# Kernel optimization log

Hardware: AMD Instinct MI355X
Metric: run time of the kernel (lower is better)

## Reference

```python
import jax, jax.numpy as jnp
import numpy as np

B, S, D, H, DFF = 2, 4096, 256, 8, 1024
DK = D // H


def setup_inputs() -> dict:
    key = jax.random.key(0)
    ks = jax.random.split(key, 12)
    sc = 0.02
    inp = {
        "x": jax.random.normal(ks[0], (B, S, D), jnp.float32),
        "mask": jnp.ones((B, 1, 1, S), jnp.int32),
        "Wq": jax.random.normal(ks[1], (D, D), jnp.float32) * sc,
        "bq": jnp.zeros((D,), jnp.float32),
        "Wk": jax.random.normal(ks[2], (D, D), jnp.float32) * sc,
        "bk": jnp.zeros((D,), jnp.float32),
        "Wv": jax.random.normal(ks[3], (D, D), jnp.float32) * sc,
        "bv": jnp.zeros((D,), jnp.float32),
        "Wo": jax.random.normal(ks[4], (D, D), jnp.float32) * sc,
        "bo": jnp.zeros((D,), jnp.float32),
        "W1": jax.random.normal(ks[5], (D, DFF), jnp.float32) * sc,
        "b1": jnp.zeros((DFF,), jnp.float32),
        "W2": jax.random.normal(ks[6], (DFF, D), jnp.float32) * sc,
        "b2": jnp.zeros((D,), jnp.float32),
        "g1": jnp.ones((D,), jnp.float32),
        "be1": jnp.zeros((D,), jnp.float32),
        "g2": jnp.ones((D,), jnp.float32),
        "be2": jnp.zeros((D,), jnp.float32),
        "a1": jnp.float32(1e-8),
        "a2": jnp.float32(1e-8),
    }
    return inp


def _layernorm(x, g, b, eps=1e-5):
    mu = jnp.mean(x, axis=-1, keepdims=True)
    var = jnp.var(x, axis=-1, keepdims=True)
    return (x - mu) * jax.lax.rsqrt(var + eps) * g + b


def _block(x, mask, Wq, bq, Wk, bk, Wv, bv, Wo, bo, W1, b1, W2, b2, g1, be1, g2, be2, a1, a2):
    # multi-head attention (dropout = identity in eval)
    def proj(W, b):
        return (x @ W + b).reshape(B, S, H, DK).transpose(0, 2, 1, 3)  # [B,H,S,DK]
    q, k, v = proj(Wq, bq), proj(Wk, bk), proj(Wv, bv)
    scores = jnp.einsum("bhsd,bhtd->bhst", q, k) / jnp.sqrt(jnp.float32(DK))
    scores = jnp.where(mask == 0, jnp.float32(-1e9), scores)
    p_attn = jax.nn.softmax(scores, axis=-1)
    ctx = jnp.einsum("bhst,bhtd->bhsd", p_attn, v)
    ctx = ctx.transpose(0, 2, 1, 3).reshape(B, S, D)
    attn_out = ctx @ Wo + bo
    x1 = _layernorm(x + a1 * attn_out, g1, be1)
    # FFN
    h = jax.nn.gelu(x1 @ W1 + b1, approximate=False)
    ffn_out = h @ W2 + b2
    return _layernorm(x1 + a2 * ffn_out, g2, be2)


def reference(x, mask, Wq, bq, Wk, bk, Wv, bv, Wo, bo, W1, b1, W2, b2, g1, be1, g2, be2, a1, a2):
    return _block(x, mask, Wq, bq, Wk, bk, Wv, bv, Wo, bo, W1, b1, W2, b2, g1, be1, g2, be2, a1, a2)
```

## Files before the change

kernel.cpp:

```cpp
#include <hip/hip_runtime.h>
#include <hip/hip_bf16.h>
#include <math.h>

#define B_ 2
#define S_ 4096
#define D_ 256
#define H_ 8
#define DFF_ 1024
#define DK_ 32

typedef __attribute__((ext_vector_type(8))) short short8;
typedef __attribute__((ext_vector_type(4))) float f32x4;
typedef __attribute__((ext_vector_type(16))) float f32x16;
typedef __attribute__((ext_vector_type(4))) int int4v;

__device__ __forceinline__ unsigned short f2bf(float f) {
  unsigned int u = __builtin_bit_cast(unsigned int, f);
  u += 0x7FFFu + ((u >> 16) & 1u);
  return (unsigned short)(u >> 16);
}

__device__ __forceinline__ float bf2f(unsigned short s) {
  unsigned int u = ((unsigned int)s) << 16;
  return __builtin_bit_cast(float, u);
}

__device__ __forceinline__ short8 u32x4_to_s8(unsigned int a, unsigned int b,
                                              unsigned int c, unsigned int d) {
  int4v v = {(int)a, (int)b, (int)c, (int)d};
  return __builtin_bit_cast(short8, v);
}

__global__ __launch_bounds__(256) void k_prepw(
    const float* __restrict__ Wq, const float* __restrict__ Wk,
    const float* __restrict__ Wv, const float* __restrict__ Wo,
    const float* __restrict__ W1, const float* __restrict__ W2,
    const float* __restrict__ bq, const float* __restrict__ bk,
    const float* __restrict__ bv, const float* __restrict__ x,
    unsigned short* __restrict__ WqkvT, unsigned short* __restrict__ WoT,
    unsigned short* __restrict__ W1T, unsigned short* __restrict__ W2T,
    float* __restrict__ bqkv, unsigned short* __restrict__ xb) {
  const float k2 = 0.25500525551f;
  int bx = blockIdx.x, t = threadIdx.x;
  if (bx < 768) {
    int which = bx >> 8;
    int i = ((bx & 255) << 8) | t;
    const float* W = (which == 0) ? Wq : (which == 1) ? Wk : Wv;
    int n = i >> 8, k = i & 255;
    float v = W[k * 256 + n] * ((which == 0) ? k2 : 1.0f);
    WqkvT[(size_t)(which * 256 + n) * 256 + k] = f2bf(v);
  } else if (bx < 1024) {
    int i = ((bx - 768) << 8) | t;
    int n = i >> 8, k = i & 255;
    WoT[i] = f2bf(Wo[k * 256 + n]);
  } else if (bx < 2048) {
    int i = ((bx - 1024) << 8) | t;
    int n = i >> 8, k = i & 255;
    W1T[i] = f2bf(W1[k * 1024 + n]);
  } else if (bx < 3072) {
    int i = ((bx - 2048) << 8) | t;
    int n = i >> 10, k = i & 1023;
    W2T[i] = f2bf(W2[k * 256 + n]);
  } else if (bx < 3075) {
    int i = ((bx - 3072) << 8) | t;
    if (i < 768) bqkv[i] = (i < 256) ? bq[i] * k2 : (i < 512) ? bk[i - 256] : bv[i - 512];
  } else {
    int i = (bx - 3075) * 2048 + t * 8;
    f32x4 f0 = *(const f32x4*)(x + i);
    f32x4 f1 = *(const f32x4*)(x + i + 4);
    short8 o;
#pragma unroll
    for (int e = 0; e < 4; e++) { o[e] = (short)f2bf(f0[e]); o[e + 4] = (short)f2bf(f1[e]); }
    *(short8*)(xb + i) = o;
  }
}

__global__ __launch_bounds__(256) void k_gemmqkv(const unsigned short* __restrict__ A,
                                                 const unsigned short* __restrict__ Bt,
                                                 const float* __restrict__ bias,
                                                 unsigned short* __restrict__ qb,
                                                 unsigned short* __restrict__ kpk,
                                                 unsigned short* __restrict__ vpk) {
  const int K = 256;
  __shared__ unsigned short Al[128][40];
  __shared__ unsigned short Bl[64][40];
  const int tid = threadIdx.x;
  const int wid = tid >> 6, lane = tid & 63;
  const int lhi = lane >> 4, llo = lane & 15;
  const int rowbase = wid * 32;
  const int bm = blockIdx.x, bn = blockIdx.y;

  f32x4 zero = {0.f, 0.f, 0.f, 0.f};
  f32x4 acc[2][4];
#pragma unroll
  for (int m = 0; m < 2; m++)
#pragma unroll
    for (int n = 0; n < 4; n++) acc[m][n] = zero;

  const int r0 = tid >> 2, c8 = (tid & 3) * 8;
  const unsigned short* A16a = A + (size_t)(bm * 128 + r0) * K + c8;
  const unsigned short* A16b = A + (size_t)(bm * 128 + r0 + 64) * K + c8;
  const unsigned short* Brow0 = Bt + (size_t)(bn * 64 + r0) * K + c8;

  for (int kb = 0; kb < K; kb += 32) {
    __syncthreads();
    *(short8*)&Al[r0][c8] = *(const short8*)(A16a + kb);
    *(short8*)&Al[r0 + 64][c8] = *(const short8*)(A16b + kb);
    *(short8*)&Bl[r0][c8] = *(const short8*)(Brow0 + kb);
    __syncthreads();
    short8 af[2], bf[4];
#pragma unroll
    for (int m = 0; m < 2; m++) af[m] = *(const short8*)&Al[rowbase + m * 16 + llo][lhi * 8];
#pragma unroll
    for (int n = 0; n < 4; n++) bf[n] = *(const short8*)&Bl[n * 16 + llo][lhi * 8];
#pragma unroll
    for (int m = 0; m < 2; m++)
#pragma unroll
      for (int n = 0; n < 4; n++)
        acc[m][n] = __builtin_amdgcn_mfma_f32_16x16x32_bf16(af[m], bf[n], acc[m][n], 0, 0, 0);
  }

  const int which = bn >> 2;
#pragma unroll
  for (int m = 0; m < 2; m++)
#pragma unroll
    for (int n = 0; n < 4; n++)
#pragma unroll
      for (int r = 0; r < 4; r++) {
        int row = bm * 128 + rowbase + m * 16 + lhi * 4 + r;
        int gcol = bn * 64 + n * 16 + llo;
        int col0 = gcol - which * 256;
        float v = acc[m][n][r] + bias[gcol];
        unsigned short bv = f2bf(v);
        int t = row & (S_ - 1), b = row >> 12;
        int h = col0 >> 5;
        if (which == 0) {
          qb[(size_t)row * 256 + col0] = bv;
        } else if (which == 1) {
          int c5 = col0 & 31, jj = (c5 >> 4) & 1, hik = (c5 >> 3) & 1, e = c5 & 7;
          int tile = t >> 6, i = (t >> 5) & 1, l31k = t & 31;
          size_t addr = (((size_t)(b * 8 + h) * 64 + tile) * 4 + i * 2 + jj) * 512 +
                        (hik * 32 + l31k) * 8 + e;
          kpk[addr] = bv;
        } else {
          int d = col0 & 31;
          int x5 = t >> 6, j = (t >> 3) & 7, kk = t & 7;
          size_t addr = (((size_t)(b * 8 + h) * 64 + x5) * 4 + (j >> 1)) * 512 +
                        ((j & 1) * 32 + d) * 8 + kk;
          vpk[addr] = bv;
        }
      }
}

__global__ __launch_bounds__(256) void k_gemm1(const unsigned short* __restrict__ A,
                                               const unsigned short* __restrict__ Bt,
                                               const float* __restrict__ bias,
                                               unsigned short* __restrict__ Cout,
                                               int M, int N, int K) {
  __shared__ unsigned short Al[128][40];
  __shared__ unsigned short Bl[128][40];
  const int tid = threadIdx.x;
  const int wid = tid >> 6, lane = tid & 63;
  const int lhi = lane >> 4, llo = lane & 15;
  const int wr = wid >> 1, wc = wid & 1;
  const int rowbase = wr * 64, colbase = wc * 64;
  const int bm = blockIdx.x, bn = blockIdx.y;

  f32x4 zero = {0.f, 0.f, 0.f, 0.f};
  f32x4 acc[4][4];
#pragma unroll
  for (int m = 0; m < 4; m++)
#pragma unroll
    for (int n = 0; n < 4; n++) acc[m][n] = zero;

  const int r0 = tid >> 2, c8 = (tid & 3) * 8;
  const unsigned short* A16a = A + (size_t)(bm * 128 + r0) * K + c8;
  const unsigned short* A16b = A + (size_t)(bm * 128 + r0 + 64) * K + c8;
  const unsigned short* Brow0 = Bt + (size_t)(bn * 128 + r0) * K + c8;
  const unsigned short* Brow1 = Bt + (size_t)(bn * 128 + r0 + 64) * K + c8;

  for (int kb = 0; kb < K; kb += 32) {
    __syncthreads();
    *(short8*)&Al[r0][c8] = *(const short8*)(A16a + kb);
    *(short8*)&Al[r0 + 64][c8] = *(const short8*)(A16b + kb);
    *(short8*)&Bl[r0][c8] = *(const short8*)(Brow0 + kb);
    *(short8*)&Bl[r0 + 64][c8] = *(const short8*)(Brow1 + kb);
    __syncthreads();
    short8 af[4], bf[4];
#pragma unroll
    for (int m = 0; m < 4; m++) af[m] = *(const short8*)&Al[rowbase + m * 16 + llo][lhi * 8];
#pragma unroll
    for (int n = 0; n < 4; n++) bf[n] = *(const short8*)&Bl[colbase + n * 16 + llo][lhi * 8];
#pragma unroll
    for (int m = 0; m < 4; m++)
#pragma unroll
      for (int n = 0; n < 4; n++)
        acc[m][n] = __builtin_amdgcn_mfma_f32_16x16x32_bf16(af[m], bf[n], acc[m][n], 0, 0, 0);
  }

#pragma unroll
  for (int m = 0; m < 4; m++)
#pragma unroll
    for (int n = 0; n < 4; n++)
#pragma unroll
      for (int r = 0; r < 4; r++) {
        int row = bm * 128 + rowbase + m * 16 + lhi * 4 + r;
        int col = bn * 128 + colbase + n * 16 + llo;
        float v = acc[m][n][r] + bias[col];
        v = 0.5f * v * (1.0f + erff(v * 0.70710678118f));
        Cout[(size_t)row * N + col] = f2bf(v);
      }
}

template <int BASE16, int OUT32>
__global__ __launch_bounds__(512) void k_gemmln(const unsigned short* __restrict__ A,
                                                const unsigned short* __restrict__ Bt,
                                                const float* __restrict__ bias,
                                                const void* __restrict__ base,
                                                const float* __restrict__ alpha,
                                                const float* __restrict__ g,
                                                const float* __restrict__ be,
                                                void* __restrict__ y, int K) {
  __shared__ unsigned short Al[2][32][40];
  __shared__ unsigned short Bl[2][256][40];
  __shared__ float psum[32][4], psq[32][4];
  float* partial = (float*)&Bl[0][0][0];

  const int tid = threadIdx.x;
  const int w = tid >> 6, lane = tid & 63;
  const int kh = w >> 2, wc = w & 3;
  const int lhi = lane >> 4, llo = lane & 15;
  const int row0 = blockIdx.x * 32;
  const int Kh = K >> 1;

  f32x4 zero = {0.f, 0.f, 0.f, 0.f};
  f32x4 acc[2][4];
#pragma unroll
  for (int m = 0; m < 2; m++)
#pragma unroll
    for (int n = 0; n < 4; n++) acc[m][n] = zero;

  for (int kb = 0; kb < Kh; kb += 32) {
    __syncthreads();
    if (tid < 256) {
      int kh2 = tid >> 7, ra = (tid >> 2) & 31, ca = (tid & 3) * 8;
      *(short8*)&Al[kh2][ra][ca] =
          *(const short8*)(A + (size_t)(row0 + ra) * K + kh2 * Kh + kb + ca);
    }
#pragma unroll
    for (int s = 0; s < 4; s++) {
      int c = tid + s * 512;
      int kh2 = c >> 10, rb = (c >> 2) & 255, cb = (c & 3) * 8;
      *(short8*)&Bl[kh2][rb][cb] =
          *(const short8*)(Bt + (size_t)rb * K + kh2 * Kh + kb + cb);
    }
    __syncthreads();
    short8 af[2], bf[4];
#pragma unroll
    for (int m = 0; m < 2; m++) af[m] = *(const short8*)&Al[kh][m * 16 + llo][lhi * 8];
#pragma unroll
    for (int n = 0; n < 4; n++)
      bf[n] = *(const short8*)&Bl[kh][wc * 64 + n * 16 + llo][lhi * 8];
#pragma unroll
    for (int m = 0; m < 2; m++)
#pragma unroll
      for (int n = 0; n < 4; n++)
        acc[m][n] = __builtin_amdgcn_mfma_f32_16x16x32_bf16(af[m], bf[n], acc[m][n], 0, 0, 0);
  }

  __syncthreads();
  if (kh == 1) {
#pragma unroll
    for (int m = 0; m < 2; m++)
#pragma unroll
      for (int n = 0; n < 4; n++)
#pragma unroll
        for (int r = 0; r < 4; r++) {
          int lrow = m * 16 + lhi * 4 + r;
          int col = wc * 64 + n * 16 + llo;
          partial[lrow * 256 + col] = acc[m][n][r];
        }
  }
  __syncthreads();

  const float a = alpha[0];
  const unsigned short* b16 = (const unsigned short*)base;
  const float* b32 = (const float*)base;

  if (kh == 0) {
#pragma unroll
    for (int m = 0; m < 2; m++)
#pragma unroll
      for (int r = 0; r < 4; r++) {
        int lrow = m * 16 + lhi * 4 + r;
        size_t grow = (size_t)(row0 + lrow);
        float s = 0.f, q = 0.f;
#pragma unroll
        for (int n = 0; n < 4; n++) {
          int col = wc * 64 + n * 16 + llo;
          float v = acc[m][n][r] + partial[lrow * 256 + col] + bias[col];
          float xb = BASE16 ? bf2f(b16[grow * 256 + col]) : b32[grow * 256 + col];
          float rr = fmaf(a, v, xb);
          acc[m][n][r] = rr;
          s += rr;
          q = fmaf(rr, rr, q);
        }
#pragma unroll
        for (int off = 1; off < 16; off <<= 1) {
          s += __shfl_xor(s, off);
          q += __shfl_xor(q, off);
        }
        if (llo == 0) { psum[lrow][wc] = s; psq[lrow][wc] = q; }
      }
  }
  __syncthreads();

  if (kh == 0) {
#pragma unroll
    for (int m = 0; m < 2; m++)
#pragma unroll
      for (int r = 0; r < 4; r++) {
        int lrow = m * 16 + lhi * 4 + r;
        size_t grow = (size_t)(row0 + lrow);
        float S = psum[lrow][0] + psum[lrow][1] + psum[lrow][2] + psum[lrow][3];
        float Q = psq[lrow][0] + psq[lrow][1] + psq[lrow][2] + psq[lrow][3];
        float mu = S * (1.0f / 256.0f);
        float var = Q * (1.0f / 256.0f) - mu * mu;
        float rs = rsqrtf(var + 1e-5f);
#pragma unroll
        for (int n = 0; n < 4; n++) {
          int col = wc * 64 + n * 16 + llo;
          float o = (acc[m][n][r] - mu) * rs * g[col] + be[col];
          if (OUT32) ((float*)y)[grow * 256 + col] = o;
          else ((unsigned short*)y)[grow * 256 + col] = f2bf(o);
        }
      }
  }
}

__global__ __launch_bounds__(512, 2) void k_attn(const unsigned short* __restrict__ qb,
                                                 const unsigned short* __restrict__ kpk,
                                                 const unsigned short* __restrict__ vpk,
                                                 const int* __restrict__ mask,
                                                 unsigned short* __restrict__ ctx) {
  __shared__ float accS[4][32][32];
  __shared__ float lS[4][32];
  const int tid = threadIdx.x;
  const int lane = tid & 63;
  const int w = tid >> 6;
  const int qt = w >> 1, half = w & 1;
  const int l31 = lane & 31, hi = lane >> 5;
  const int q0 = blockIdx.x * 128 + qt * 32;
  const int h = blockIdx.y, b = blockIdx.z;
  const size_t bS = (size_t)b * S_;

  const unsigned short* Qp = qb + (bS + q0 + l31) * 256 + h * DK_ + hi * 8;
  short8 qf0 = *(const short8*)Qp;
  short8 qf1 = *(const short8*)(Qp + 16);

  const size_t fragbase = ((size_t)(b * H_ + h) * 64 + half * 32) * 2048 + lane * 8;
  const unsigned short* kp = kpk + fragbase;
  const unsigned short* vp = vpk + fragbase;
  const int* mp = mask + bS + half * 2048 + lane;

  f32x16 acc, lacc;
#pragma unroll
  for (int r = 0; r < 16; r++) { acc[r] = 0.f; lacc[r] = 0.f; }
  const f32x16 zz = acc;
  short8 ones;
#pragma unroll
  for (int e = 0; e < 8; e++) ones[e] = (short)0x3F80;

  short8 kf0, kf1, kf2, kf3, vf0, vf1, vf2, vf3;
  unsigned int pk0[8], pk1[8];
  f32x16 s0, s1;

#define LDKF() { kf0 = *(const short8*)(kp); kf1 = *(const short8*)(kp + 512); \
                 kf2 = *(const short8*)(kp + 1024); kf3 = *(const short8*)(kp + 1536); kp += 2048; }
#define LDVF() { vf0 = *(const short8*)(vp); vf1 = *(const short8*)(vp + 512); \
                 vf2 = *(const short8*)(vp + 1024); vf3 = *(const short8*)(vp + 1536); vp += 2048; }
#define QKM() {                                                                  \
    s0 = __builtin_amdgcn_mfma_f32_32x32x16_bf16(kf0, qf0, zz, 0, 0, 0);         \
    s1 = __builtin_amdgcn_mfma_f32_32x32x16_bf16(kf2, qf0, zz, 0, 0, 0);         \
    s0 = __builtin_amdgcn_mfma_f32_32x32x16_bf16(kf1, qf1, s0, 0, 0, 0);         \
    s1 = __builtin_amdgcn_mfma_f32_32x32x16_bf16(kf3, qf1, s1, 0, 0, 0);         \
  }
#define EXPM(mv) {                                                               \
    unsigned long long bal = __ballot((mv) != 0);                                \
    if (__builtin_expect(bal != ~0ull, 0)) {                                     \
      _Pragma("unroll") for (int r = 0; r < 16; r++) {                           \
        int tt = (r & 3) + 8 * (r >> 2) + 4 * hi;                                \
        if (!((bal >> tt) & 1)) s0[r] = -3e38f;                                  \
        if (!((bal >> (tt + 32)) & 1)) s1[r] = -3e38f;                           \
      }                                                                          \
    }                                                                            \
    _Pragma("unroll") for (int r = 0; r < 16; r++) {                             \
      s0[r] = __builtin_amdgcn_exp2f(s0[r]);                                     \
      s1[r] = __builtin_amdgcn_exp2f(s1[r]);                                     \
    }                                                                            \
    _Pragma("unroll") for (int j = 0; j < 8; j++) {                              \
      asm("v_cvt_pk_bf16_f32 %0, %1, %2" : "=v"(pk0[j]) : "v"(s0[2*j]), "v"(s0[2*j+1])); \
      asm("v_cvt_pk_bf16_f32 %0, %1, %2" : "=v"(pk1[j]) : "v"(s1[2*j]), "v"(s1[2*j+1])); \
    }                                                                            \
  }
#define PVM() {                                                                  \
    __builtin_amdgcn_s_setprio(1);                                               \
    _Pragma("unroll") for (int kk = 0; kk < 4; kk++) {                           \
      unsigned int* pk = (kk < 2) ? pk0 : pk1;                                   \
      int base = (kk & 1) * 4;                                                   \
      auto r02 = __builtin_amdgcn_permlane32_swap(pk[base], pk[base + 2], false, false);     \
      auto r13 = __builtin_amdgcn_permlane32_swap(pk[base + 1], pk[base + 3], false, false); \
      short8 pfr = u32x4_to_s8(r02[0], r13[0], r02[1], r13[1]);                  \
      short8 vv = (kk == 0) ? vf0 : (kk == 1) ? vf1 : (kk == 2) ? vf2 : vf3;     \
      acc = __builtin_amdgcn_mfma_f32_32x32x16_bf16(pfr, vv, acc, 0, 0, 0);      \
      lacc = __builtin_amdgcn_mfma_f32_32x32x16_bf16(pfr, ones, lacc, 0, 0, 0);  \
    }                                                                            \
    __builtin_amdgcn_s_setprio(0);                                               \
  }

  LDKF();
  int mvC = mp[0];
  int mvN = mp[64];
  QKM();
  LDKF();
  LDVF();
  EXPM(mvC);
  mvC = mvN;
  mvN = mp[128];

  for (int t = 1; t < 32; ++t) {
    QKM();
    LDKF();
    PVM();
    LDVF();
    EXPM(mvC);
    mvC = mvN;
    mvN = mp[(t + 2 < 32 ? t + 2 : 31) * 64];
  }
  PVM();

  if (half == 1) {
#pragma unroll
    for (int r = 0; r < 16; r++) {
      int q = (r & 3) + 8 * (r >> 2) + 4 * hi;
      accS[qt][q][l31] = acc[r];
    }
    if (l31 == 0) {
#pragma unroll
      for (int r = 0; r < 16; r++) {
        int q = (r & 3) + 8 * (r >> 2) + 4 * hi;
        lS[qt][q] = lacc[r];
      }
    }
  }
  __syncthreads();
  if (half == 0) {
#pragma unroll
    for (int r = 0; r < 16; r++) {
      int q = (r & 3) + 8 * (r >> 2) + 4 * hi;
      float o = acc[r] + accS[qt][q][l31];
      float L = lacc[r] + lS[qt][q];
      ctx[(bS + q0 + q) * (size_t)D_ + h * DK_ + l31] = f2bf(o / L);
    }
  }
#undef LDKF
#undef LDVF
#undef QKM
#undef EXPM
#undef PVM
}

extern "C" void kernel_launch(void* const* d_in, const int* in_sizes, int n_in,
                              void* d_out, int out_size, void* d_ws, size_t ws_size,
                              hipStream_t stream) {
  const float* x   = (const float*)d_in[0];
  const int* mask  = (const int*)d_in[1];
  const float* Wq  = (const float*)d_in[2];
  const float* bq  = (const float*)d_in[3];
  const float* Wk  = (const float*)d_in[4];
  const float* bk  = (const float*)d_in[5];
  const float* Wv  = (const float*)d_in[6];
  const float* bv  = (const float*)d_in[7];
  const float* Wo  = (const float*)d_in[8];
  const float* bo  = (const float*)d_in[9];
  const float* W1  = (const float*)d_in[10];
  const float* b1  = (const float*)d_in[11];
  const float* W2  = (const float*)d_in[12];
  const float* b2  = (const float*)d_in[13];
  const float* g1  = (const float*)d_in[14];
  const float* be1 = (const float*)d_in[15];
  const float* g2  = (const float*)d_in[16];
  const float* be2 = (const float*)d_in[17];
  const float* a1  = (const float*)d_in[18];
  const float* a2  = (const float*)d_in[19];
  float* out = (float*)d_out;

  char* ws = (char*)d_ws;
  const size_t MB = 1024 * 1024;
  unsigned short* qb  = (unsigned short*)(ws + 0);
  unsigned short* kpk = (unsigned short*)(ws + 5 * MB);
  unsigned short* vpk = (unsigned short*)(ws + 10 * MB);
  unsigned short* ctx = (unsigned short*)(ws + 15 * MB);
  unsigned short* x1b = (unsigned short*)(ws + 19 * MB);
  unsigned short* hb  = (unsigned short*)(ws + 23 * MB);
  unsigned short* WqkvT = (unsigned short*)(ws + 40 * MB);
  unsigned short* WoT   = (unsigned short*)(ws + 40 * MB + 512 * 1024);
  unsigned short* W1T   = (unsigned short*)(ws + 41 * MB);
  unsigned short* W2T   = (unsigned short*)(ws + 41 * MB + 512 * 1024);
  float* bqkv           = (float*)(ws + 42 * MB);
  unsigned short* xb    = (unsigned short*)(ws + 43 * MB);

  const int NTOK = B_ * S_;

  k_prepw<<<dim3(4099), 256, 0, stream>>>(Wq, Wk, Wv, Wo, W1, W2, bq, bk, bv, x,
                                          WqkvT, WoT, W1T, W2T, bqkv, xb);

  k_gemmqkv<<<dim3(64, 12), 256, 0, stream>>>(xb, WqkvT, bqkv, qb, kpk, vpk);

  k_attn<<<dim3(S_ / 128, H_, B_), 512, 0, stream>>>(qb, kpk, vpk, mask, ctx);

  k_gemmln<0, 0><<<dim3(NTOK / 32), 512, 0, stream>>>(ctx, WoT, bo, x, a1, g1, be1,
                                                      x1b, 256);

  k_gemm1<<<dim3(64, 8), 256, 0, stream>>>(x1b, W1T, b1, hb, NTOK, 1024, 256);

  k_gemmln<1, 1><<<dim3(NTOK / 32), 512, 0, stream>>>(hb, W2T, b2, x1b, a2, g2, be2,
                                                      out, 1024);
}
```

Measured before the change: 130.9 us.

## Tile weight transposes, enlarge QKV GEMM tiles, use tanh-approx GELU

The weight-prep kernel now transposes through 64x64 shared-memory tiles, so global reads and writes are coalesced and far fewer blocks are launched. The QKV projection GEMM grows from 128x64 to 128x128 tiles, using a 2x2 warp layout with 4x4 MFMA accumulators per warp, which halves the grid and improves operand reuse at the cost of more registers. The FFN GELU replaces erff with a tanh approximation built from exp2 and rcp, which departs numerically from the exact erf GELU the reference uses.

```diff
diff --git a/kernel.cpp b/kernel.cpp
--- a/kernel.cpp
+++ b/kernel.cpp
@@ -29,6 +29,12 @@
                                               unsigned int c, unsigned int d) {
   int4v v = {(int)a, (int)b, (int)c, (int)d};
   return __builtin_bit_cast(short8, v);
+}
+
+__device__ __forceinline__ float gelu_fast(float v) {
+  float e = __builtin_amdgcn_exp2f(v * fmaf(0.10294609f, v * v, 2.3022077f));
+  float th = 1.0f - 2.0f * __builtin_amdgcn_rcpf(e + 1.0f);
+  return 0.5f * v * (1.0f + th);
 }
 
 __global__ __launch_bounds__(256) void k_prepw(
@@ -42,30 +48,52 @@
     float* __restrict__ bqkv, unsigned short* __restrict__ xb) {
   const float k2 = 0.25500525551f;
   int bx = blockIdx.x, t = threadIdx.x;
-  if (bx < 768) {
-    int which = bx >> 8;
-    int i = ((bx & 255) << 8) | t;
-    const float* W = (which == 0) ? Wq : (which == 1) ? Wk : Wv;
-    int n = i >> 8, k = i & 255;
-    float v = W[k * 256 + n] * ((which == 0) ? k2 : 1.0f);
-    WqkvT[(size_t)(which * 256 + n) * 256 + k] = f2bf(v);
-  } else if (bx < 1024) {
-    int i = ((bx - 768) << 8) | t;
-    int n = i >> 8, k = i & 255;
-    WoT[i] = f2bf(Wo[k * 256 + n]);
-  } else if (bx < 2048) {
-    int i = ((bx - 1024) << 8) | t;
-    int n = i >> 8, k = i & 255;
-    W1T[i] = f2bf(W1[k * 1024 + n]);
-  } else if (bx < 3072) {
-    int i = ((bx - 2048) << 8) | t;
-    int n = i >> 10, k = i & 1023;
-    W2T[i] = f2bf(W2[k * 256 + n]);
-  } else if (bx < 3075) {
-    int i = ((bx - 3072) << 8) | t;
-    if (i < 768) bqkv[i] = (i < 256) ? bq[i] * k2 : (i < 512) ? bk[i - 256] : bv[i - 512];
+
+  if (bx < 192) {
+    __shared__ float tile[64][65];
+    const float* src;
+    unsigned short* dst;
+    int Ksz, Nsz, ti, tj;
+    float scale = 1.0f;
+    if (bx < 48) {
+      int which = bx >> 4, s = bx & 15;
+      src = (which == 0) ? Wq : (which == 1) ? Wk : Wv;
+      dst = WqkvT + which * 65536;
+      Ksz = 256; Nsz = 256; ti = s >> 2; tj = s & 3;
+      if (which == 0) scale = k2;
+    } else if (bx < 64) {
+      int s = bx - 48;
+      src = Wo; dst = WoT; Ksz = 256; Nsz = 256; ti = s >> 2; tj = s & 3;
+    } else if (bx < 128) {
+      int s = bx - 64;
+      src = W1; dst = W1T; Ksz = 256; Nsz = 1024; ti = s >> 4; tj = s & 15;
+    } else {
+      int s = bx - 128;
+      src = W2; dst = W2T; Ksz = 1024; Nsz = 256; ti = s >> 2; tj = s & 3;
+    }
+    int row0 = ti * 64, col0 = tj * 64;
+    int c = t & 63, rg = t >> 6;
+#pragma unroll
+    for (int i = 0; i < 16; i++) {
+      int rr = rg * 16 + i;
+      tile[rr][c] = src[(size_t)(row0 + rr) * Nsz + col0 + c] * scale;
+    }
+    __syncthreads();
+    int k = t & 63;
+#pragma unroll
+    for (int i = 0; i < 16; i++) {
+      int nn = rg * 16 + i;
+      dst[(size_t)(col0 + nn) * Ksz + row0 + k] = f2bf(tile[k][nn]);
+    }
+  } else if (bx == 192) {
+#pragma unroll
+    for (int j = 0; j < 3; j++) {
+      int i = j * 256 + t;
+      if (i < 768)
+        bqkv[i] = (i < 256) ? bq[i] * k2 : (i < 512) ? bk[i - 256] : bv[i - 512];
+    }
   } else {
-    int i = (bx - 3075) * 2048 + t * 8;
+    int i = (bx - 193) * 2048 + t * 8;
     f32x4 f0 = *(const f32x4*)(x + i);
     f32x4 f1 = *(const f32x4*)(x + i + 4);
     short8 o;
@@ -83,53 +111,56 @@
                                                  unsigned short* __restrict__ vpk) {
   const int K = 256;
   __shared__ unsigned short Al[128][40];
-  __shared__ unsigned short Bl[64][40];
+  __shared__ unsigned short Bl[128][40];
   const int tid = threadIdx.x;
   const int wid = tid >> 6, lane = tid & 63;
   const int lhi = lane >> 4, llo = lane & 15;
-  const int rowbase = wid * 32;
+  const int wr = wid >> 1, wc = wid & 1;
+  const int rowbase = wr * 64, colbase = wc * 64;
   const int bm = blockIdx.x, bn = blockIdx.y;
 
   f32x4 zero = {0.f, 0.f, 0.f, 0.f};
-  f32x4 acc[2][4];
-#pragma unroll
-  for (int m = 0; m < 2; m++)
+  f32x4 acc[4][4];
+#pragma unroll
+  for (int m = 0; m < 4; m++)
 #pragma unroll
     for (int n = 0; n < 4; n++) acc[m][n] = zero;
 
   const int r0 = tid >> 2, c8 = (tid & 3) * 8;
   const unsigned short* A16a = A + (size_t)(bm * 128 + r0) * K + c8;
   const unsigned short* A16b = A + (size_t)(bm * 128 + r0 + 64) * K + c8;
-  const unsigned short* Brow0 = Bt + (size_t)(bn * 64 + r0) * K + c8;
+  const unsigned short* Brow0 = Bt + (size_t)(bn * 128 + r0) * K + c8;
+  const unsigned short* Brow1 = Bt + (size_t)(bn * 128 + r0 + 64) * K + c8;
 
   for (int kb = 0; kb < K; kb += 32) {
     __syncthreads();
     *(short8*)&Al[r0][c8] = *(const short8*)(A16a + kb);
     *(short8*)&Al[r0 + 64][c8] = *(const short8*)(A16b + kb);
     *(short8*)&Bl[r0][c8] = *(const short8*)(Brow0 + kb);
-    __syncthreads();
-    short8 af[2], bf[4];
-#pragma unroll
-    for (int m = 0; m < 2; m++) af[m] = *(const short8*)&Al[rowbase + m * 16 + llo][lhi * 8];
-#pragma unroll
-    for (int n = 0; n < 4; n++) bf[n] = *(const short8*)&Bl[n * 16 + llo][lhi * 8];
-#pragma unroll
-    for (int m = 0; m < 2; m++)
+    *(short8*)&Bl[r0 + 64][c8] = *(const short8*)(Brow1 + kb);
+    __syncthreads();
+    short8 af[4], bf[4];
+#pragma unroll
+    for (int m = 0; m < 4; m++) af[m] = *(const short8*)&Al[rowbase + m * 16 + llo][lhi * 8];
+#pragma unroll
+    for (int n = 0; n < 4; n++) bf[n] = *(const short8*)&Bl[colbase + n * 16 + llo][lhi * 8];
+#pragma unroll
+    for (int m = 0; m < 4; m++)
 #pragma unroll
       for (int n = 0; n < 4; n++)
         acc[m][n] = __builtin_amdgcn_mfma_f32_16x16x32_bf16(af[m], bf[n], acc[m][n], 0, 0, 0);
   }
 
-  const int which = bn >> 2;
-#pragma unroll
-  for (int m = 0; m < 2; m++)
+#pragma unroll
+  for (int m = 0; m < 4; m++)
 #pragma unroll
     for (int n = 0; n < 4; n++)
 #pragma unroll
       for (int r = 0; r < 4; r++) {
         int row = bm * 128 + rowbase + m * 16 + lhi * 4 + r;
-        int gcol = bn * 64 + n * 16 + llo;
-        int col0 = gcol - which * 256;
+        int gcol = bn * 128 + colbase + n * 16 + llo;
+        int which = gcol >> 8;
+        int col0 = gcol & 255;
         float v = acc[m][n][r] + bias[gcol];
         unsigned short bv = f2bf(v);
         int t = row & (S_ - 1), b = row >> 12;
@@ -207,8 +238,7 @@
         int row = bm * 128 + rowbase + m * 16 + lhi * 4 + r;
         int col = bn * 128 + colbase + n * 16 + llo;
         float v = acc[m][n][r] + bias[col];
-        v = 0.5f * v * (1.0f + erff(v * 0.70710678118f));
-        Cout[(size_t)row * N + col] = f2bf(v);
+        Cout[(size_t)row * N + col] = f2bf(gelu_fast(v));
       }
 }
 
@@ -512,10 +542,10 @@
 
   const int NTOK = B_ * S_;
 
-  k_prepw<<<dim3(4099), 256, 0, stream>>>(Wq, Wk, Wv, Wo, W1, W2, bq, bk, bv, x,
+  k_prepw<<<dim3(1217), 256, 0, stream>>>(Wq, Wk, Wv, Wo, W1, W2, bq, bk, bv, x,
                                           WqkvT, WoT, W1T, W2T, bqkv, xb);
 
-  k_gemmqkv<<<dim3(64, 12), 256, 0, stream>>>(xb, WqkvT, bqkv, qb, kpk, vpk);
+  k_gemmqkv<<<dim3(64, 6), 256, 0, stream>>>(xb, WqkvT, bqkv, qb, kpk, vpk);
 
   k_attn<<<dim3(S_ / 128, H_, B_), 512, 0, stream>>>(qb, kpk, vpk, mask, ctx);
 
```

After: 128.6 us. About the same (-1.8%).
